# Optimization experiments

Hardware: AMD Instinct MI355X
Metric: run time of the kernel (lower is better)

Reference implementation:

```python
import jax, jax.numpy as jnp
import numpy as np

B, S, H, D = 16, 2048, 768, 128
ATTR_MAX, ITEMS_MAX = 8, 32  # static equivalents of attr_type_ids.max() / item_position_ids max (data generated to hit these)


def setup_inputs() -> dict:
    key = jax.random.key(0)
    k1, k2, k3, k4 = jax.random.split(key, 4)
    return {
        "attention_mask": jnp.ones((B, S), dtype=jnp.int32),
        "hidden_states": jax.random.normal(k1, (B, S, H), dtype=jnp.float32),
        "attr_type_ids": jax.random.randint(k2, (B, S), 0, ATTR_MAX + 1),
        "item_position_ids": jax.random.randint(k3, (B, S), 0, ITEMS_MAX + 1),
        "W": jax.random.normal(k4, (H, D), dtype=jnp.float32) * (1.0 / np.sqrt(H)),
        "b": jnp.zeros((D,), dtype=jnp.float32),
    }


def reference(attention_mask, hidden_states, attr_type_ids, item_position_ids, W, b):
    # linear projection: [B,S,H] @ [H,D] -> [B,S,D]
    h = jnp.einsum('bsh,hd->bsd', hidden_states, W) + b
    Bn, Sn, Dn = h.shape

    # segmented mean over (attr_id, item_id) groups; attr/item id 0 (and >max, e.g. the 50 pad sentinel) are invalid
    valid = (attr_type_ids >= 1) & (attr_type_ids <= ATTR_MAX) & \
            (item_position_ids >= 1) & (item_position_ids <= ITEMS_MAX)
    batch_idx = jnp.arange(Bn)[:, None]
    seg = (batch_idx * ATTR_MAX + (attr_type_ids - 1)) * ITEMS_MAX + (item_position_ids - 1)
    nseg = Bn * ATTR_MAX * ITEMS_MAX
    seg = jnp.where(valid, seg, nseg)  # dump invalid tokens into extra segment
    flat_seg = seg.reshape(-1)

    sums = jax.ops.segment_sum(h.reshape(-1, Dn), flat_seg, num_segments=nseg + 1)[:nseg]
    counts = jax.ops.segment_sum(valid.reshape(-1).astype(h.dtype), flat_seg, num_segments=nseg + 1)[:nseg]

    sums = sums.reshape(Bn, ATTR_MAX, ITEMS_MAX, Dn)
    counts = counts.reshape(Bn, ATTR_MAX, ITEMS_MAX)
    empty = counts == 0
    pooled = sums / jnp.where(empty, jnp.ones_like(counts), counts)[..., None]
    return pooled, empty, h
```

## Files before the change

### kernel.cpp

```cpp
#include <hip/hip_runtime.h>
#include <hip/hip_bf16.h>

#define Bn 16
#define Sn 2048
#define Hn 768
#define Dn 128
#define AT 8
#define IT 32
#define NSEG (Bn*AT*IT)

typedef __attribute__((ext_vector_type(4))) float f32x4;
typedef __attribute__((ext_vector_type(4))) int   i32x4;
typedef __attribute__((ext_vector_type(8))) short bf16x8;
typedef __attribute__((ext_vector_type(4))) short s16x4;

__device__ __forceinline__ unsigned short f2bf(float f){
  __hip_bfloat16 h = __float2bfloat16(f);
  return *reinterpret_cast<unsigned short*>(&h);
}

__global__ __launch_bounds__(256) void k_prep(const float* __restrict__ W,
                                              unsigned short* __restrict__ Wt){
  __shared__ float sT[64][65];
  const int tid = threadIdx.x;
  const int k0 = (blockIdx.x % 12) * 64;
  const int d0 = (blockIdx.x / 12) * 64;
  const int rr = tid >> 4;
  const int cg = tid & 15;

  #pragma unroll
  for (int p = 0; p < 4; ++p){
    int k = rr + p*16;
    f32x4 v = *(const f32x4*)&W[(size_t)(k0 + k)*Dn + d0 + cg*4];
    sT[k][cg*4+0] = v[0]; sT[k][cg*4+1] = v[1];
    sT[k][cg*4+2] = v[2]; sT[k][cg*4+3] = v[3];
  }
  __syncthreads();
  #pragma unroll
  for (int p = 0; p < 4; ++p){
    int d = rr + p*16;
    s16x4 t;
    #pragma unroll
    for (int j = 0; j < 4; ++j) t[j] = (short)f2bf(sT[cg*4+j][d]);
    *(s16x4*)&Wt[(size_t)(d0 + d)*Hn + k0 + cg*4] = t;
  }
}

__global__ __launch_bounds__(256, 4) void k_gemm(const float* __restrict__ X,
        const unsigned short* __restrict__ Wt, const float* __restrict__ bias,
        float* __restrict__ Hout){
  __shared__ unsigned char sA[2][32*128];
  __shared__ unsigned char sB[2][128*128];
  const int tid  = threadIdx.x;
  const int lane = tid & 63;
  const int wave = tid >> 6;
  const int m0 = blockIdx.x * 32;

  const int ar = tid >> 3, ak = tid & 7;
  const int bc = tid >> 1, bkh = tid & 1;
  const float*          Ap = X  + (size_t)(m0 + ar)*Hn + ak*8;
  const unsigned short* Bp = Wt + (size_t)bc*Hn + bkh*32;

  int aw[2], bw[4];
  #pragma unroll
  for (int c=0;c<2;c++) aw[c] = ar*128 + ((ak*16 + c*8) ^ ((ar&7)<<4));
  #pragma unroll
  for (int c=0;c<4;c++) bw[c] = bc*128 + ((bkh*64 + c*16) ^ ((bc&7)<<4));

  int abase[2], aswz[2];
  #pragma unroll
  for (int mi=0;mi<2;mi++){
    int row = mi*16 + (lane&15);
    abase[mi] = row*128; aswz[mi] = (row&7)<<4;
  }
  int bbase[2], bswz[2];
  #pragma unroll
  for (int ni=0;ni<2;ni++){
    int col = wave*32 + ni*16 + (lane&15);
    bbase[ni] = col*128; bswz[ni] = (col&7)<<4;
  }
  const int kblk = (lane>>4)*16;

  f32x4 acc[2][2];
  #pragma unroll
  for (int mi=0;mi<2;mi++)
    #pragma unroll
    for (int ni=0;ni<2;ni++) acc[mi][ni] = (f32x4){0.f,0.f,0.f,0.f};

  f32x4 av[2]; i32x4 bv[4];
  #pragma unroll
  for (int c=0;c<2;c++) av[c] = *(const f32x4*)(Ap + c*4);
  #pragma unroll
  for (int c=0;c<4;c++) bv[c] = *(const i32x4*)(Bp + c*8);
  #pragma unroll
  for (int c=0;c<2;c++){
    s16x4 t;
    t[0]=(short)f2bf(av[c][0]); t[1]=(short)f2bf(av[c][1]);
    t[2]=(short)f2bf(av[c][2]); t[3]=(short)f2bf(av[c][3]);
    *(s16x4*)&sA[0][aw[c]] = t;
  }
  #pragma unroll
  for (int c=0;c<4;c++) *(i32x4*)&sB[0][bw[c]] = bv[c];
  __syncthreads();

  int cur = 0;
  #pragma unroll
  for (int step=0; step<12; ++step){
    if (step < 11){
      #pragma unroll
      for (int c=0;c<2;c++) av[c] = *(const f32x4*)(Ap + (step+1)*64 + c*4);
      #pragma unroll
      for (int c=0;c<4;c++) bv[c] = *(const i32x4*)(Bp + (step+1)*64 + c*8);
    }
    #pragma unroll
    for (int ks=0; ks<2; ++ks){
      bf16x8 af[2], bfv[2];
      #pragma unroll
      for (int mi=0;mi<2;mi++)
        af[mi] = *(const bf16x8*)&sA[cur][abase[mi] + ((ks*64 + kblk) ^ aswz[mi])];
      #pragma unroll
      for (int ni=0;ni<2;ni++)
        bfv[ni] = *(const bf16x8*)&sB[cur][bbase[ni] + ((ks*64 + kblk) ^ bswz[ni])];
      #pragma unroll
      for (int mi=0;mi<2;mi++)
        #pragma unroll
        for (int ni=0;ni<2;ni++)
          acc[mi][ni] = __builtin_amdgcn_mfma_f32_16x16x32_bf16(af[mi], bfv[ni], acc[mi][ni], 0, 0, 0);
    }
    if (step < 11){
      #pragma unroll
      for (int c=0;c<2;c++){
        s16x4 t;
        t[0]=(short)f2bf(av[c][0]); t[1]=(short)f2bf(av[c][1]);
        t[2]=(short)f2bf(av[c][2]); t[3]=(short)f2bf(av[c][3]);
        *(s16x4*)&sA[cur^1][aw[c]] = t;
      }
      #pragma unroll
      for (int c=0;c<4;c++) *(i32x4*)&sB[cur^1][bw[c]] = bv[c];
    }
    __syncthreads();
    cur ^= 1;
  }

  #pragma unroll
  for (int ni=0;ni<2;ni++){
    int col = wave*32 + ni*16 + (lane&15);
    float bb = bias[col];
    #pragma unroll
    for (int mi=0;mi<2;mi++){
      int row0 = m0 + mi*16 + (lane>>4)*4;
      #pragma unroll
      for (int r=0;r<4;r++)
        Hout[(size_t)(row0 + r)*Dn + col] = acc[mi][ni][r] + bb;
    }
  }
}

__global__ __launch_bounds__(256) void k_scan(const int* __restrict__ attr,
        const int* __restrict__ item, const float* __restrict__ Hsrc,
        float* __restrict__ pooled, float* __restrict__ empty){
  __shared__ float ssum[4][IT][64];
  __shared__ int   slist[4][512];
  __shared__ int   scnt[IT];

  const int wg  = blockIdx.x;
  const int dh  = wg & 1;
  const int a   = (wg >> 1) & 7;
  const int b   = wg >> 4;
  const int tid = threadIdx.x;
  const int wv  = tid >> 6;
  const int lane = tid & 63;

  #pragma unroll
  for (int i = 0; i < IT; ++i) ssum[wv][i][lane] = 0.f;
  if (tid < IT) scnt[tid] = 0;

  const int tok0 = wv * 512;
  const int gbase = b * Sn;
  int nm = 0;
  #pragma unroll
  for (int g = 0; g < 8; ++g){
    int tok = tok0 + g*64 + lane;
    int avv = attr[gbase + tok], ivv = item[gbase + tok];
    bool m = (avv == a+1) && (ivv >= 1) && (ivv <= IT);
    unsigned long long mask = __ballot(m);
    int pos = nm + __popcll(mask & ((1ull << lane) - 1ull));
    if (m) slist[wv][pos] = ((ivv-1) << 16) | tok;
    nm += __popcll(mask);
  }
  __syncthreads();

  for (int e = lane; e < nm; e += 64) atomicAdd(&scnt[slist[wv][e] >> 16], 1);

  const float* hb = Hsrc + (size_t)b*Sn*Dn + dh*64 + lane;
  int e = 0;
  for (; e + 8 <= nm; e += 8){
    int idx[8]; float v[8];
    #pragma unroll
    for (int j=0;j<8;j++) idx[j] = slist[wv][e+j];
    #pragma unroll
    for (int j=0;j<8;j++) v[j] = hb[(size_t)(idx[j] & 0xffff)*Dn];
    #pragma unroll
    for (int j=0;j<8;j++) ssum[wv][idx[j]>>16][lane] += v[j];
  }
  for (; e < nm; ++e){
    int idx = slist[wv][e];
    ssum[wv][idx>>16][lane] += hb[(size_t)(idx & 0xffff)*Dn];
  }
  __syncthreads();

  float* outp = pooled + (size_t)(b*AT + a)*IT*Dn + dh*64;
  for (int o = tid; o < IT*64; o += 256){
    int i = o >> 6, d = o & 63;
    float s = ssum[0][i][d] + ssum[1][i][d] + ssum[2][i][d] + ssum[3][i][d];
    int cnt = scnt[i];
    outp[i*Dn + d] = s / (float)(cnt > 0 ? cnt : 1);
  }
  if (dh == 0 && tid < IT)
    empty[(b*AT + a)*IT + tid] = (scnt[tid] == 0) ? 1.f : 0.f;
}

extern "C" void kernel_launch(void* const* d_in, const int* in_sizes, int n_in,
                              void* d_out, int out_size, void* d_ws, size_t ws_size,
                              hipStream_t stream) {
  const float* hidden = (const float*)d_in[1];
  const int*   attr   = (const int*)  d_in[2];
  const int*   item   = (const int*)  d_in[3];
  const float* W      = (const float*)d_in[4];
  const float* bias   = (const float*)d_in[5];

  float* pooled = (float*)d_out;
  float* empty  = pooled + (size_t)NSEG*Dn;
  float* Hout   = empty  + NSEG;

  unsigned short* Wt = (unsigned short*)d_ws;

  k_prep<<<24, 256, 0, stream>>>(W, Wt);
  k_gemm<<<(Bn*Sn)/32, 256, 0, stream>>>(hidden, Wt, bias, Hout);
  k_scan<<<Bn*AT*2, 256, 0, stream>>>(attr, item, Hout, pooled, empty);
}
```

Measured before the change: 46.22 us.

## Load GEMM fragments directly from global memory, dropping LDS staging

The GEMM kernel no longer stages A and B tiles through double-buffered shared memory with barriers. Each wave now loads its MFMA operand fragments straight from global memory, converting A to bf16 in registers. The block tile grows from 32 to 64 rows, with waves arranged 2x2 so each wave owns a 32x64 output, and the grid halves. This removes LDS traffic and syncthreads, but it gives up cross-wave reuse through shared memory, so more global and L2 requests are issued with smaller, strided access per lane.

```diff
diff --git a/kernel.cpp b/kernel.cpp
--- a/kernel.cpp
+++ b/kernel.cpp
@@ -46,109 +46,64 @@
   }
 }
 
-__global__ __launch_bounds__(256, 4) void k_gemm(const float* __restrict__ X,
+__global__ __launch_bounds__(256) void k_gemm(const float* __restrict__ X,
         const unsigned short* __restrict__ Wt, const float* __restrict__ bias,
         float* __restrict__ Hout){
-  __shared__ unsigned char sA[2][32*128];
-  __shared__ unsigned char sB[2][128*128];
   const int tid  = threadIdx.x;
   const int lane = tid & 63;
   const int wave = tid >> 6;
-  const int m0 = blockIdx.x * 32;
+  const int wm   = wave >> 1;
+  const int wn   = wave & 1;
+  const int m0   = blockIdx.x * 64;
+  const int r16  = lane & 15;
+  const int kg   = lane >> 4;
 
-  const int ar = tid >> 3, ak = tid & 7;
-  const int bc = tid >> 1, bkh = tid & 1;
-  const float*          Ap = X  + (size_t)(m0 + ar)*Hn + ak*8;
-  const unsigned short* Bp = Wt + (size_t)bc*Hn + bkh*32;
+  const float* Ap[2];
+  #pragma unroll
+  for (int mi=0;mi<2;mi++)
+    Ap[mi] = X + (size_t)(m0 + wm*32 + mi*16 + r16)*Hn + kg*8;
+  const unsigned short* Bp[4];
+  #pragma unroll
+  for (int ni=0;ni<4;ni++)
+    Bp[ni] = Wt + (size_t)(wn*64 + ni*16 + r16)*Hn + kg*8;
 
-  int aw[2], bw[4];
-  #pragma unroll
-  for (int c=0;c<2;c++) aw[c] = ar*128 + ((ak*16 + c*8) ^ ((ar&7)<<4));
-  #pragma unroll
-  for (int c=0;c<4;c++) bw[c] = bc*128 + ((bkh*64 + c*16) ^ ((bc&7)<<4));
-
-  int abase[2], aswz[2];
-  #pragma unroll
-  for (int mi=0;mi<2;mi++){
-    int row = mi*16 + (lane&15);
-    abase[mi] = row*128; aswz[mi] = (row&7)<<4;
-  }
-  int bbase[2], bswz[2];
-  #pragma unroll
-  for (int ni=0;ni<2;ni++){
-    int col = wave*32 + ni*16 + (lane&15);
-    bbase[ni] = col*128; bswz[ni] = (col&7)<<4;
-  }
-  const int kblk = (lane>>4)*16;
-
-  f32x4 acc[2][2];
+  f32x4 acc[2][4];
   #pragma unroll
   for (int mi=0;mi<2;mi++)
     #pragma unroll
-    for (int ni=0;ni<2;ni++) acc[mi][ni] = (f32x4){0.f,0.f,0.f,0.f};
+    for (int ni=0;ni<4;ni++) acc[mi][ni] = (f32x4){0.f,0.f,0.f,0.f};
 
-  f32x4 av[2]; i32x4 bv[4];
-  #pragma unroll
-  for (int c=0;c<2;c++) av[c] = *(const f32x4*)(Ap + c*4);
-  #pragma unroll
-  for (int c=0;c<4;c++) bv[c] = *(const i32x4*)(Bp + c*8);
-  #pragma unroll
-  for (int c=0;c<2;c++){
-    s16x4 t;
-    t[0]=(short)f2bf(av[c][0]); t[1]=(short)f2bf(av[c][1]);
-    t[2]=(short)f2bf(av[c][2]); t[3]=(short)f2bf(av[c][3]);
-    *(s16x4*)&sA[0][aw[c]] = t;
-  }
-  #pragma unroll
-  for (int c=0;c<4;c++) *(i32x4*)&sB[0][bw[c]] = bv[c];
-  __syncthreads();
-
-  int cur = 0;
-  #pragma unroll
-  for (int step=0; step<12; ++step){
-    if (step < 11){
-      #pragma unroll
-      for (int c=0;c<2;c++) av[c] = *(const f32x4*)(Ap + (step+1)*64 + c*4);
-      #pragma unroll
-      for (int c=0;c<4;c++) bv[c] = *(const i32x4*)(Bp + (step+1)*64 + c*8);
+  #pragma unroll 4
+  for (int step=0; step<24; ++step){
+    const int koff = step*32;
+    bf16x8 a[2], b[4];
+    #pragma unroll
+    for (int mi=0;mi<2;mi++){
+      f32x4 lo = *(const f32x4*)(Ap[mi] + koff);
+      f32x4 hi = *(const f32x4*)(Ap[mi] + koff + 4);
+      bf16x8 t;
+      t[0]=(short)f2bf(lo[0]); t[1]=(short)f2bf(lo[1]);
+      t[2]=(short)f2bf(lo[2]); t[3]=(short)f2bf(lo[3]);
+      t[4]=(short)f2bf(hi[0]); t[5]=(short)f2bf(hi[1]);
+      t[6]=(short)f2bf(hi[2]); t[7]=(short)f2bf(hi[3]);
+      a[mi] = t;
     }
     #pragma unroll
-    for (int ks=0; ks<2; ++ks){
-      bf16x8 af[2], bfv[2];
+    for (int ni=0;ni<4;ni++) b[ni] = *(const bf16x8*)(Bp[ni] + koff);
+    #pragma unroll
+    for (int mi=0;mi<2;mi++)
       #pragma unroll
-      for (int mi=0;mi<2;mi++)
-        af[mi] = *(const bf16x8*)&sA[cur][abase[mi] + ((ks*64 + kblk) ^ aswz[mi])];
-      #pragma unroll
-      for (int ni=0;ni<2;ni++)
-        bfv[ni] = *(const bf16x8*)&sB[cur][bbase[ni] + ((ks*64 + kblk) ^ bswz[ni])];
-      #pragma unroll
-      for (int mi=0;mi<2;mi++)
-        #pragma unroll
-        for (int ni=0;ni<2;ni++)
-          acc[mi][ni] = __builtin_amdgcn_mfma_f32_16x16x32_bf16(af[mi], bfv[ni], acc[mi][ni], 0, 0, 0);
-    }
-    if (step < 11){
-      #pragma unroll
-      for (int c=0;c<2;c++){
-        s16x4 t;
-        t[0]=(short)f2bf(av[c][0]); t[1]=(short)f2bf(av[c][1]);
-        t[2]=(short)f2bf(av[c][2]); t[3]=(short)f2bf(av[c][3]);
-        *(s16x4*)&sA[cur^1][aw[c]] = t;
-      }
-      #pragma unroll
-      for (int c=0;c<4;c++) *(i32x4*)&sB[cur^1][bw[c]] = bv[c];
-    }
-    __syncthreads();
-    cur ^= 1;
+      for (int ni=0;ni<4;ni++)
+        acc[mi][ni] = __builtin_amdgcn_mfma_f32_16x16x32_bf16(a[mi], b[ni], acc[mi][ni], 0, 0, 0);
   }
 
   #pragma unroll
-  for (int ni=0;ni<2;ni++){
-    int col = wave*32 + ni*16 + (lane&15);
+  for (int ni=0;ni<4;ni++){
+    int col = wn*64 + ni*16 + r16;
     float bb = bias[col];
     #pragma unroll
     for (int mi=0;mi<2;mi++){
-      int row0 = m0 + mi*16 + (lane>>4)*4;
+      int row0 = m0 + wm*32 + mi*16 + kg*4;
       #pragma unroll
       for (int r=0;r<4;r++)
         Hout[(size_t)(row0 + r)*Dn + col] = acc[mi][ni][r] + bb;
@@ -236,6 +191,6 @@
   unsigned short* Wt = (unsigned short*)d_ws;
 
   k_prep<<<24, 256, 0, stream>>>(W, Wt);
-  k_gemm<<<(Bn*Sn)/32, 256, 0, stream>>>(hidden, Wt, bias, Hout);
+  k_gemm<<<(Bn*Sn)/64, 256, 0, stream>>>(hidden, Wt, bias, Hout);
   k_scan<<<Bn*AT*2, 256, 0, stream>>>(attr, item, Hout, pooled, empty);
 }
```

New measurement: 68.28 us. 47.7% more time.
